# Performance work log

Measured on AMD Instinct MI355X. Metric: run time of the kernel, lower is better.

## Reference

```python
import jax, jax.numpy as jnp
import numpy as np

B, H, W, C, NH, K = 4, 56, 56, 128, 4, 7


def setup_inputs() -> dict:
    key = jax.random.key(0)
    ks = jax.random.split(key, 6)
    x = jax.random.normal(ks[0], (B, H, W, C), dtype=jnp.float32)
    w_qkv = jax.random.normal(ks[1], (C, 3 * C), dtype=jnp.float32) * 0.02
    b_qkv = jnp.zeros((3 * C,), dtype=jnp.float32)
    rpb = jax.random.normal(ks[2], (NH, 2 * K - 1, 2 * K - 1), dtype=jnp.float32) * 0.02
    w_proj = jax.random.normal(ks[3], (C, C), dtype=jnp.float32) * 0.02
    b_proj = jnp.zeros((C,), dtype=jnp.float32)
    return {"x": x, "w_qkv": w_qkv, "b_qkv": b_qkv, "rpb": rpb,
            "w_proj": w_proj, "b_proj": b_proj}


def reference(x, w_qkv, b_qkv, rpb, w_proj, b_proj):
    B_, H_, W_, C_ = x.shape
    nh = rpb.shape[0]
    k = (rpb.shape[1] + 1) // 2          # kernel_size
    hd = C_ // nh                        # head_dim
    nb = k // 2                          # neighborhood radius
    scale = hd ** -0.5

    qkv = (x @ w_qkv + b_qkv).reshape(B_, H_, W_, 3, nh, hd)
    q = qkv[:, :, :, 0].transpose(0, 3, 1, 2, 4) * scale   # [B,nh,H,W,hd]
    kk = qkv[:, :, :, 1].transpose(0, 3, 1, 2, 4)          # [B,nh,H,W,hd]
    v = qkv[:, :, :, 2].transpose(0, 3, 1, 2, 4)           # [B,nh,H,W,hd]

    # NATTEN window start indices: window clamped to stay in-bounds (query shifts off-center at edges)
    si = jnp.clip(jnp.arange(H_) - nb, 0, H_ - k)          # [H]
    sj = jnp.clip(jnp.arange(W_) - nb, 0, W_ - k)          # [W]
    idx_i = si[:, None] + jnp.arange(k)                    # [H,k] absolute key rows
    idx_j = sj[:, None] + jnp.arange(k)                    # [W,k] absolute key cols

    # gather neighborhood keys/values: [B,nh,H,k,W,k,hd] (axes: b n i p j q d)
    k_win = kk[:, :, idx_i][:, :, :, :, idx_j]
    v_win = v[:, :, idx_i][:, :, :, :, idx_j]

    # relative position bias: index = key_pos - query_pos + (k-1)
    rel_i = idx_i - jnp.arange(H_)[:, None] + (k - 1)      # [H,k]
    rel_j = idx_j - jnp.arange(W_)[:, None] + (k - 1)      # [W,k]
    bias = rpb[:, rel_i][:, :, :, rel_j]                   # [nh,H,k,W,k]
    bias = bias.transpose(0, 1, 3, 2, 4)                   # [nh,H,W,k,k]

    attn = jnp.einsum('bnijd,bnipjqd->bnijpq', q, k_win) + bias[None]
    attn = jax.nn.softmax(attn.reshape(B_, nh, H_, W_, k * k), axis=-1)
    attn = attn.reshape(B_, nh, H_, W_, k, k)

    out = jnp.einsum('bnijpq,bnipjqd->bnijd', attn, v_win)  # [B,nh,H,W,hd]
    out = out.transpose(0, 2, 3, 1, 4).reshape(B_, H_, W_, C_)
    return out @ w_proj + b_proj
```

## Files before the change

### kernel.cpp

```cpp
#include <hip/hip_runtime.h>

#define BATCH 4
#define HH 56
#define WW 56
#define CC 128
#define NHD 4
#define HD 32
#define KS 7
#define NB 3
#define HWSZ (HH * WW)
#define RPBW 13
#define QKV_N 384
#define QKV_ELE ((size_t)BATCH * NHD * HWSZ * HD)

__global__ __launch_bounds__(256) void qkv_gemm(
    const float* __restrict__ x, const float* __restrict__ w,
    const float* __restrict__ bias,
    float* __restrict__ qb, float* __restrict__ kb, float* __restrict__ vb)
{
    __shared__ float As[32][68];
    __shared__ float Bs[32][132];

    const int tid = threadIdx.x;
    const int tx  = tid & 15;
    const int ty  = tid >> 4;
    const int m0  = blockIdx.x * 64;
    const int n0  = blockIdx.y * 128;

    float acc[4][8];
    {
        const float4 ba = *(const float4*)(bias + n0 + 4 * tx);
        const float4 bb = *(const float4*)(bias + n0 + 64 + 4 * tx);
        #pragma unroll
        for (int i = 0; i < 4; ++i) {
            acc[i][0] = ba.x; acc[i][1] = ba.y; acc[i][2] = ba.z; acc[i][3] = ba.w;
            acc[i][4] = bb.x; acc[i][5] = bb.y; acc[i][6] = bb.z; acc[i][7] = bb.w;
        }
    }

    for (int kc = 0; kc < 128; kc += 32) {
        #pragma unroll
        for (int t = tid; t < 512; t += 256) {
            const int row = t >> 3;
            const int k4  = t & 7;
            const float4 xv = *(const float4*)(x + (size_t)(m0 + row) * CC + kc + 4 * k4);
            As[4 * k4 + 0][row] = xv.x;
            As[4 * k4 + 1][row] = xv.y;
            As[4 * k4 + 2][row] = xv.z;
            As[4 * k4 + 3][row] = xv.w;
        }
        #pragma unroll
        for (int t = tid; t < 1024; t += 256) {
            const int kr = t >> 5;
            const int n4 = t & 31;
            *(float4*)&Bs[kr][4 * n4] =
                *(const float4*)(w + (size_t)(kc + kr) * QKV_N + n0 + 4 * n4);
        }
        __syncthreads();
        #pragma unroll
        for (int kk = 0; kk < 32; ++kk) {
            const float4 a0 = *(const float4*)&As[kk][4 * ty];
            const float4 b0 = *(const float4*)&Bs[kk][4 * tx];
            const float4 b1 = *(const float4*)&Bs[kk][64 + 4 * tx];
            const float av[4] = {a0.x, a0.y, a0.z, a0.w};
            const float bv[8] = {b0.x, b0.y, b0.z, b0.w, b1.x, b1.y, b1.z, b1.w};
            #pragma unroll
            for (int i = 0; i < 4; ++i)
                #pragma unroll
                for (int j = 0; j < 8; ++j)
                    acc[i][j] += av[i] * bv[j];
        }
        __syncthreads();
    }

    const int t     = n0 >> 7;
    float* dst      = (t == 0) ? qb : (t == 1) ? kb : vb;
    const float scl = (t == 0) ? 0.17677669529663687f : 1.0f;
    const int c0 = 4 * tx;
    const int c1 = 64 + 4 * tx;
    const int h0 = c0 >> 5, d0 = c0 & 31;
    const int h1 = c1 >> 5, d1 = c1 & 31;
    const int b  = m0 / HWSZ;
    #pragma unroll
    for (int i = 0; i < 4; ++i) {
        const int m  = m0 + 4 * ty + i;
        const int ij = m - b * HWSZ;
        float* p0 = dst + ((size_t)(b * NHD + h0) * HWSZ + ij) * HD + d0;
        float* p1 = dst + ((size_t)(b * NHD + h1) * HWSZ + ij) * HD + d1;
        *(float4*)p0 = make_float4(acc[i][0] * scl, acc[i][1] * scl,
                                   acc[i][2] * scl, acc[i][3] * scl);
        *(float4*)p1 = make_float4(acc[i][4] * scl, acc[i][5] * scl,
                                   acc[i][6] * scl, acc[i][7] * scl);
    }
}

__global__ __launch_bounds__(256) void natten_attn(
    const float* __restrict__ qb, const float* __restrict__ kb,
    const float* __restrict__ vb, const float* __restrict__ rpb,
    float* __restrict__ ob)
{
    __shared__ float4 Ks[8][197];
    __shared__ float4 Vs[8][197];
    __shared__ float rpbs[RPBW * RPBW];

    const int tid = threadIdx.x;
    const int qid = tid >> 2;
    const int sub = tid & 3;
    const int qi_l = qid >> 3;
    const int qj_l = qid & 7;
    const int ti = blockIdx.x / 7;
    const int tj = blockIdx.x % 7;
    const int head = blockIdx.y;
    const int b    = blockIdx.z;
    const int qi = ti * 8 + qi_l;
    const int qj = tj * 8 + qj_l;
    const int R0 = min(max(ti * 8 - NB, 0), HH - 14);
    const int C0 = min(max(tj * 8 - NB, 0), WW - 14);

    const size_t base = (size_t)(b * NHD + head) * HWSZ;

    if (tid < RPBW * RPBW) rpbs[tid] = rpb[head * (RPBW * RPBW) + tid];

    for (int idx = tid; idx < 1568; idx += 256) {
        const int pos = idx >> 3;
        const int c   = idx & 7;
        const int ri  = pos / 14;
        const int rj  = pos - ri * 14;
        const size_t g = (base + (size_t)(R0 + ri) * WW + (C0 + rj)) * HD;
        Ks[c][pos] = ((const float4*)(kb + g))[c];
        Vs[c][pos] = ((const float4*)(vb + g))[c];
    }

    const int c0 = sub * 2;
    const float4* qp = (const float4*)(qb + (base + (size_t)qi * WW + qj) * HD) + c0;
    const float4 q0 = qp[0];
    const float4 q1 = qp[1];

    const int si  = min(max(qi - NB, 0), HH - KS);
    const int sj  = min(max(qj - NB, 0), WW - KS);
    const int ri0 = si - R0;
    const int rj0 = sj - C0;
    const int oi  = si - qi + (KS - 1);
    const int oj  = sj - qj + (KS - 1);

    __syncthreads();

    float s[49];
    #pragma unroll
    for (int pi = 0; pi < 7; ++pi) {
        const int rowoff = (ri0 + pi) * 14 + rj0;
        const int boff   = (oi + pi) * RPBW + oj;
        #pragma unroll
        for (int pj = 0; pj < 7; ++pj) {
            const int pos = rowoff + pj;
            const float4 k0 = Ks[c0][pos];
            const float4 k1 = Ks[c0 + 1][pos];
            float d = q0.x * k0.x + q0.y * k0.y + q0.z * k0.z + q0.w * k0.w
                    + q1.x * k1.x + q1.y * k1.y + q1.z * k1.z + q1.w * k1.w;
            d += __shfl_xor(d, 1, 64);
            d += __shfl_xor(d, 2, 64);
            s[pi * 7 + pj] = d + rpbs[boff + pj];
        }
    }

    float m = s[0];
    #pragma unroll
    for (int p = 1; p < 49; ++p) m = fmaxf(m, s[p]);
    float l = 0.f;
    #pragma unroll
    for (int p = 0; p < 49; ++p) { s[p] = __expf(s[p] - m); l += s[p]; }
    const float inv = 1.f / l;

    float4 o0 = make_float4(0.f, 0.f, 0.f, 0.f);
    float4 o1 = make_float4(0.f, 0.f, 0.f, 0.f);
    #pragma unroll
    for (int pi = 0; pi < 7; ++pi) {
        const int rowoff = (ri0 + pi) * 14 + rj0;
        #pragma unroll
        for (int pj = 0; pj < 7; ++pj) {
            const int pos = rowoff + pj;
            const float wt = s[pi * 7 + pj];
            const float4 v0 = Vs[c0][pos];
            const float4 v1 = Vs[c0 + 1][pos];
            o0.x += wt * v0.x; o0.y += wt * v0.y; o0.z += wt * v0.z; o0.w += wt * v0.w;
            o1.x += wt * v1.x; o1.y += wt * v1.y; o1.z += wt * v1.z; o1.w += wt * v1.w;
        }
    }

    float* op = ob + ((size_t)b * HWSZ + (size_t)qi * WW + qj) * CC + head * HD + sub * 8;
    ((float4*)op)[0] = make_float4(o0.x * inv, o0.y * inv, o0.z * inv, o0.w * inv);
    ((float4*)op)[1] = make_float4(o1.x * inv, o1.y * inv, o1.z * inv, o1.w * inv);
}

__global__ __launch_bounds__(256) void proj_gemm(
    const float* __restrict__ a, const float* __restrict__ w,
    const float* __restrict__ bias, float* __restrict__ out)
{
    __shared__ float As[32][36];
    __shared__ float Bs[32][132];

    const int tid = threadIdx.x;
    const int tx  = tid & 15;
    const int ty  = tid >> 4;
    const int m0  = blockIdx.x * 32;

    float acc[2][8];
    {
        const float4 ba = *(const float4*)(bias + 4 * tx);
        const float4 bb = *(const float4*)(bias + 64 + 4 * tx);
        #pragma unroll
        for (int i = 0; i < 2; ++i) {
            acc[i][0] = ba.x; acc[i][1] = ba.y; acc[i][2] = ba.z; acc[i][3] = ba.w;
            acc[i][4] = bb.x; acc[i][5] = bb.y; acc[i][6] = bb.z; acc[i][7] = bb.w;
        }
    }

    for (int kc = 0; kc < 128; kc += 32) {
        {
            const int row = tid >> 3;
            const int k4  = tid & 7;
            const float4 xv = *(const float4*)(a + (size_t)(m0 + row) * CC + kc + 4 * k4);
            As[4 * k4 + 0][row] = xv.x;
            As[4 * k4 + 1][row] = xv.y;
            As[4 * k4 + 2][row] = xv.z;
            As[4 * k4 + 3][row] = xv.w;
        }
        #pragma unroll
        for (int t = tid; t < 1024; t += 256) {
            const int kr = t >> 5;
            const int n4 = t & 31;
            *(float4*)&Bs[kr][4 * n4] =
                *(const float4*)(w + (size_t)(kc + kr) * CC + 4 * n4);
        }
        __syncthreads();
        #pragma unroll
        for (int kk = 0; kk < 32; ++kk) {
            const float2 a0 = *(const float2*)&As[kk][2 * ty];
            const float4 b0 = *(const float4*)&Bs[kk][4 * tx];
            const float4 b1 = *(const float4*)&Bs[kk][64 + 4 * tx];
            const float av[2] = {a0.x, a0.y};
            const float bv[8] = {b0.x, b0.y, b0.z, b0.w, b1.x, b1.y, b1.z, b1.w};
            #pragma unroll
            for (int i = 0; i < 2; ++i)
                #pragma unroll
                for (int j = 0; j < 8; ++j)
                    acc[i][j] += av[i] * bv[j];
        }
        __syncthreads();
    }

    #pragma unroll
    for (int i = 0; i < 2; ++i) {
        const int m = m0 + 2 * ty + i;
        float* p = out + (size_t)m * CC;
        *(float4*)(p + 4 * tx)      = make_float4(acc[i][0], acc[i][1], acc[i][2], acc[i][3]);
        *(float4*)(p + 64 + 4 * tx) = make_float4(acc[i][4], acc[i][5], acc[i][6], acc[i][7]);
    }
}

extern "C" void kernel_launch(void* const* d_in, const int* in_sizes, int n_in,
                              void* d_out, int out_size, void* d_ws, size_t ws_size,
                              hipStream_t stream) {
    const float* x      = (const float*)d_in[0];
    const float* w_qkv  = (const float*)d_in[1];
    const float* b_qkv  = (const float*)d_in[2];
    const float* rpb    = (const float*)d_in[3];
    const float* w_proj = (const float*)d_in[4];
    const float* b_proj = (const float*)d_in[5];
    float* out = (float*)d_out;

    float* ws  = (float*)d_ws;
    float* qbf = ws;
    float* kbf = ws + QKV_ELE;
    float* vbf = ws + 2 * QKV_ELE;
    float* obf = ws + 3 * QKV_ELE;

    qkv_gemm<<<dim3(196, 3), 256, 0, stream>>>(x, w_qkv, b_qkv, qbf, kbf, vbf);
    natten_attn<<<dim3(49, NHD, BATCH), 256, 0, stream>>>(qbf, kbf, vbf, rpb, obf);
    proj_gemm<<<392, 256, 0, stream>>>(obf, w_proj, b_proj, out);
}
```

Measured before the change: 127.5 us.

## Replace shared-memory tiled GEMMs with column-per-thread register GEMMs

```diff
diff --git a/kernel.cpp b/kernel.cpp
--- a/kernel.cpp
+++ b/kernel.cpp
@@ -13,84 +13,50 @@
 #define QKV_N 384
 #define QKV_ELE ((size_t)BATCH * NHD * HWSZ * HD)
 
-__global__ __launch_bounds__(256) void qkv_gemm(
+__global__ __launch_bounds__(384) void qkv_gemm(
     const float* __restrict__ x, const float* __restrict__ w,
     const float* __restrict__ bias,
     float* __restrict__ qb, float* __restrict__ kb, float* __restrict__ vb)
 {
-    __shared__ float As[32][68];
-    __shared__ float Bs[32][132];
-
-    const int tid = threadIdx.x;
-    const int tx  = tid & 15;
-    const int ty  = tid >> 4;
-    const int m0  = blockIdx.x * 64;
-    const int n0  = blockIdx.y * 128;
-
-    float acc[4][8];
-    {
-        const float4 ba = *(const float4*)(bias + n0 + 4 * tx);
-        const float4 bb = *(const float4*)(bias + n0 + 64 + 4 * tx);
-        #pragma unroll
-        for (int i = 0; i < 4; ++i) {
-            acc[i][0] = ba.x; acc[i][1] = ba.y; acc[i][2] = ba.z; acc[i][3] = ba.w;
-            acc[i][4] = bb.x; acc[i][5] = bb.y; acc[i][6] = bb.z; acc[i][7] = bb.w;
-        }
-    }
-
-    for (int kc = 0; kc < 128; kc += 32) {
-        #pragma unroll
-        for (int t = tid; t < 512; t += 256) {
-            const int row = t >> 3;
-            const int k4  = t & 7;
-            const float4 xv = *(const float4*)(x + (size_t)(m0 + row) * CC + kc + 4 * k4);
-            As[4 * k4 + 0][row] = xv.x;
-            As[4 * k4 + 1][row] = xv.y;
-            As[4 * k4 + 2][row] = xv.z;
-            As[4 * k4 + 3][row] = xv.w;
-        }
-        #pragma unroll
-        for (int t = tid; t < 1024; t += 256) {
-            const int kr = t >> 5;
-            const int n4 = t & 31;
-            *(float4*)&Bs[kr][4 * n4] =
-                *(const float4*)(w + (size_t)(kc + kr) * QKV_N + n0 + 4 * n4);
-        }
-        __syncthreads();
-        #pragma unroll
-        for (int kk = 0; kk < 32; ++kk) {
-            const float4 a0 = *(const float4*)&As[kk][4 * ty];
-            const float4 b0 = *(const float4*)&Bs[kk][4 * tx];
-            const float4 b1 = *(const float4*)&Bs[kk][64 + 4 * tx];
-            const float av[4] = {a0.x, a0.y, a0.z, a0.w};
-            const float bv[8] = {b0.x, b0.y, b0.z, b0.w, b1.x, b1.y, b1.z, b1.w};
-            #pragma unroll
-            for (int i = 0; i < 4; ++i)
-                #pragma unroll
-                for (int j = 0; j < 8; ++j)
-                    acc[i][j] += av[i] * bv[j];
-        }
-        __syncthreads();
-    }
-
-    const int t     = n0 >> 7;
-    float* dst      = (t == 0) ? qb : (t == 1) ? kb : vb;
+    const int col = threadIdx.x;
+    const int m0  = blockIdx.x * 16;
+
+    float acc[16];
+    const float bv = bias[col];
+    #pragma unroll
+    for (int r = 0; r < 16; ++r) acc[r] = bv;
+
+    const float* xrow = x + (size_t)m0 * CC;
+    const float* wc   = w + col;
+
+    for (int k4 = 0; k4 < 32; ++k4) {
+        const float w0 = wc[(k4 * 4 + 0) * QKV_N];
+        const float w1 = wc[(k4 * 4 + 1) * QKV_N];
+        const float w2 = wc[(k4 * 4 + 2) * QKV_N];
+        const float w3 = wc[(k4 * 4 + 3) * QKV_N];
+        #pragma unroll
+        for (int r = 0; r < 16; ++r) {
+            const float4 xv = *(const float4*)(xrow + (size_t)r * CC + k4 * 4);
+            acc[r] = fmaf(xv.x, w0, acc[r]);
+            acc[r] = fmaf(xv.y, w1, acc[r]);
+            acc[r] = fmaf(xv.z, w2, acc[r]);
+            acc[r] = fmaf(xv.w, w3, acc[r]);
+        }
+    }
+
+    const int t    = col >> 7;
+    const int rem  = col & 127;
+    const int head = rem >> 5;
+    const int d    = rem & 31;
     const float scl = (t == 0) ? 0.17677669529663687f : 1.0f;
-    const int c0 = 4 * tx;
-    const int c1 = 64 + 4 * tx;
-    const int h0 = c0 >> 5, d0 = c0 & 31;
-    const int h1 = c1 >> 5, d1 = c1 & 31;
-    const int b  = m0 / HWSZ;
-    #pragma unroll
-    for (int i = 0; i < 4; ++i) {
-        const int m  = m0 + 4 * ty + i;
-        const int ij = m - b * HWSZ;
-        float* p0 = dst + ((size_t)(b * NHD + h0) * HWSZ + ij) * HD + d0;
-        float* p1 = dst + ((size_t)(b * NHD + h1) * HWSZ + ij) * HD + d1;
-        *(float4*)p0 = make_float4(acc[i][0] * scl, acc[i][1] * scl,
-                                   acc[i][2] * scl, acc[i][3] * scl);
-        *(float4*)p1 = make_float4(acc[i][4] * scl, acc[i][5] * scl,
-                                   acc[i][6] * scl, acc[i][7] * scl);
+    float* dst = (t == 0) ? qb : (t == 1) ? kb : vb;
+
+    const int b   = m0 / HWSZ;
+    const int ij0 = m0 - b * HWSZ;
+    float* dsth = dst + (size_t)(b * NHD + head) * HWSZ * HD + d;
+    #pragma unroll
+    for (int r = 0; r < 16; ++r) {
+        dsth[(size_t)(ij0 + r) * HD] = acc[r] * scl;
     }
 }
 
@@ -192,70 +158,39 @@
     ((float4*)op)[1] = make_float4(o1.x * inv, o1.y * inv, o1.z * inv, o1.w * inv);
 }
 
-__global__ __launch_bounds__(256) void proj_gemm(
+__global__ __launch_bounds__(128) void proj_gemm(
     const float* __restrict__ a, const float* __restrict__ w,
     const float* __restrict__ bias, float* __restrict__ out)
 {
-    __shared__ float As[32][36];
-    __shared__ float Bs[32][132];
-
-    const int tid = threadIdx.x;
-    const int tx  = tid & 15;
-    const int ty  = tid >> 4;
-    const int m0  = blockIdx.x * 32;
-
-    float acc[2][8];
-    {
-        const float4 ba = *(const float4*)(bias + 4 * tx);
-        const float4 bb = *(const float4*)(bias + 64 + 4 * tx);
-        #pragma unroll
-        for (int i = 0; i < 2; ++i) {
-            acc[i][0] = ba.x; acc[i][1] = ba.y; acc[i][2] = ba.z; acc[i][3] = ba.w;
-            acc[i][4] = bb.x; acc[i][5] = bb.y; acc[i][6] = bb.z; acc[i][7] = bb.w;
-        }
-    }
-
-    for (int kc = 0; kc < 128; kc += 32) {
-        {
-            const int row = tid >> 3;
-            const int k4  = tid & 7;
-            const float4 xv = *(const float4*)(a + (size_t)(m0 + row) * CC + kc + 4 * k4);
-            As[4 * k4 + 0][row] = xv.x;
-            As[4 * k4 + 1][row] = xv.y;
-            As[4 * k4 + 2][row] = xv.z;
-            As[4 * k4 + 3][row] = xv.w;
-        }
-        #pragma unroll
-        for (int t = tid; t < 1024; t += 256) {
-            const int kr = t >> 5;
-            const int n4 = t & 31;
-            *(float4*)&Bs[kr][4 * n4] =
-                *(const float4*)(w + (size_t)(kc + kr) * CC + 4 * n4);
-        }
-        __syncthreads();
-        #pragma unroll
-        for (int kk = 0; kk < 32; ++kk) {
-            const float2 a0 = *(const float2*)&As[kk][2 * ty];
-            const float4 b0 = *(const float4*)&Bs[kk][4 * tx];
-            const float4 b1 = *(const float4*)&Bs[kk][64 + 4 * tx];
-            const float av[2] = {a0.x, a0.y};
-            const float bv[8] = {b0.x, b0.y, b0.z, b0.w, b1.x, b1.y, b1.z, b1.w};
-            #pragma unroll
-            for (int i = 0; i < 2; ++i)
-                #pragma unroll
-                for (int j = 0; j < 8; ++j)
-                    acc[i][j] += av[i] * bv[j];
-        }
-        __syncthreads();
-    }
-
-    #pragma unroll
-    for (int i = 0; i < 2; ++i) {
-        const int m = m0 + 2 * ty + i;
-        float* p = out + (size_t)m * CC;
-        *(float4*)(p + 4 * tx)      = make_float4(acc[i][0], acc[i][1], acc[i][2], acc[i][3]);
-        *(float4*)(p + 64 + 4 * tx) = make_float4(acc[i][4], acc[i][5], acc[i][6], acc[i][7]);
-    }
+    const int col = threadIdx.x;
+    const int m0  = blockIdx.x * 16;
+
+    float acc[16];
+    const float bv = bias[col];
+    #pragma unroll
+    for (int r = 0; r < 16; ++r) acc[r] = bv;
+
+    const float* arow = a + (size_t)m0 * CC;
+    const float* wc   = w + col;
+
+    for (int k4 = 0; k4 < 32; ++k4) {
+        const float w0 = wc[(k4 * 4 + 0) * CC];
+        const float w1 = wc[(k4 * 4 + 1) * CC];
+        const float w2 = wc[(k4 * 4 + 2) * CC];
+        const float w3 = wc[(k4 * 4 + 3) * CC];
+        #pragma unroll
+        for (int r = 0; r < 16; ++r) {
+            const float4 av = *(const float4*)(arow + (size_t)r * CC + k4 * 4);
+            acc[r] = fmaf(av.x, w0, acc[r]);
+            acc[r] = fmaf(av.y, w1, acc[r]);
+            acc[r] = fmaf(av.z, w2, acc[r]);
+            acc[r] = fmaf(av.w, w3, acc[r]);
+        }
+    }
+
+    float* op = out + (size_t)m0 * CC + col;
+    #pragma unroll
+    for (int r = 0; r < 16; ++r) op[(size_t)r * CC] = acc[r];
 }
 
 extern "C" void kernel_launch(void* const* d_in, const int* in_sizes, int n_in,
@@ -275,7 +210,7 @@
     float* vbf = ws + 2 * QKV_ELE;
     float* obf = ws + 3 * QKV_ELE;
 
-    qkv_gemm<<<dim3(196, 3), 256, 0, stream>>>(x, w_qkv, b_qkv, qbf, kbf, vbf);
+    qkv_gemm<<<784, 384, 0, stream>>>(x, w_qkv, b_qkv, qbf, kbf, vbf);
     natten_attn<<<dim3(49, NHD, BATCH), 256, 0, stream>>>(qbf, kbf, vbf, rpb, obf);
-    proj_gemm<<<392, 256, 0, stream>>>(obf, w_proj, b_proj, out);
-}
+    proj_gemm<<<784, 128, 0, stream>>>(obf, w_proj, b_proj, out);
+}
```

New measurement: 148.3 us. 1.16x slower.

## Load full A tile once and stream weights directly from global in GEMMs

Applied to the files above, without the earlier changes.

```diff
diff --git a/kernel.cpp b/kernel.cpp
--- a/kernel.cpp
+++ b/kernel.cpp
@@ -18,8 +18,7 @@
     const float* __restrict__ bias,
     float* __restrict__ qb, float* __restrict__ kb, float* __restrict__ vb)
 {
-    __shared__ float As[32][68];
-    __shared__ float Bs[32][132];
+    __shared__ float As[128][68];
 
     const int tid = threadIdx.x;
     const int tx  = tid & 15;
@@ -27,6 +26,17 @@
     const int m0  = blockIdx.x * 64;
     const int n0  = blockIdx.y * 128;
 
+    #pragma unroll
+    for (int t = tid; t < 2048; t += 256) {
+        const int row = t >> 5;
+        const int k4  = t & 31;
+        const float4 xv = *(const float4*)(x + (size_t)(m0 + row) * CC + 4 * k4);
+        As[4 * k4 + 0][row] = xv.x;
+        As[4 * k4 + 1][row] = xv.y;
+        As[4 * k4 + 2][row] = xv.z;
+        As[4 * k4 + 3][row] = xv.w;
+    }
+
     float acc[4][8];
     {
         const float4 ba = *(const float4*)(bias + n0 + 4 * tx);
@@ -38,39 +48,22 @@
         }
     }
 
-    for (int kc = 0; kc < 128; kc += 32) {
-        #pragma unroll
-        for (int t = tid; t < 512; t += 256) {
-            const int row = t >> 3;
-            const int k4  = t & 7;
-            const float4 xv = *(const float4*)(x + (size_t)(m0 + row) * CC + kc + 4 * k4);
-            As[4 * k4 + 0][row] = xv.x;
-            As[4 * k4 + 1][row] = xv.y;
-            As[4 * k4 + 2][row] = xv.z;
-            As[4 * k4 + 3][row] = xv.w;
-        }
-        #pragma unroll
-        for (int t = tid; t < 1024; t += 256) {
-            const int kr = t >> 5;
-            const int n4 = t & 31;
-            *(float4*)&Bs[kr][4 * n4] =
-                *(const float4*)(w + (size_t)(kc + kr) * QKV_N + n0 + 4 * n4);
-        }
-        __syncthreads();
-        #pragma unroll
-        for (int kk = 0; kk < 32; ++kk) {
-            const float4 a0 = *(const float4*)&As[kk][4 * ty];
-            const float4 b0 = *(const float4*)&Bs[kk][4 * tx];
-            const float4 b1 = *(const float4*)&Bs[kk][64 + 4 * tx];
-            const float av[4] = {a0.x, a0.y, a0.z, a0.w};
-            const float bv[8] = {b0.x, b0.y, b0.z, b0.w, b1.x, b1.y, b1.z, b1.w};
+    __syncthreads();
+
+    const float* wp0 = w + n0 + 4 * tx;
+    const float* wp1 = w + n0 + 64 + 4 * tx;
+    #pragma unroll 4
+    for (int kk = 0; kk < 128; ++kk) {
+        const float4 b0 = *(const float4*)(wp0 + (size_t)kk * QKV_N);
+        const float4 b1 = *(const float4*)(wp1 + (size_t)kk * QKV_N);
+        const float4 a0 = *(const float4*)&As[kk][4 * ty];
+        const float av[4] = {a0.x, a0.y, a0.z, a0.w};
+        const float bv[8] = {b0.x, b0.y, b0.z, b0.w, b1.x, b1.y, b1.z, b1.w};
+        #pragma unroll
+        for (int i = 0; i < 4; ++i)
             #pragma unroll
-            for (int i = 0; i < 4; ++i)
-                #pragma unroll
-                for (int j = 0; j < 8; ++j)
-                    acc[i][j] += av[i] * bv[j];
-        }
-        __syncthreads();
+            for (int j = 0; j < 8; ++j)
+                acc[i][j] = fmaf(av[i], bv[j], acc[i][j]);
     }
 
     const int t     = n0 >> 7;
@@ -196,14 +189,24 @@
     const float* __restrict__ a, const float* __restrict__ w,
     const float* __restrict__ bias, float* __restrict__ out)
 {
-    __shared__ float As[32][36];
-    __shared__ float Bs[32][132];
+    __shared__ float As[128][36];
 
     const int tid = threadIdx.x;
     const int tx  = tid & 15;
     const int ty  = tid >> 4;
     const int m0  = blockIdx.x * 32;
 
+    #pragma unroll
+    for (int t = tid; t < 1024; t += 256) {
+        const int row = t >> 5;
+        const int k4  = t & 31;
+        const float4 xv = *(const float4*)(a + (size_t)(m0 + row) * CC + 4 * k4);
+        As[4 * k4 + 0][row] = xv.x;
+        As[4 * k4 + 1][row] = xv.y;
+        As[4 * k4 + 2][row] = xv.z;
+        As[4 * k4 + 3][row] = xv.w;
+    }
+
     float acc[2][8];
     {
         const float4 ba = *(const float4*)(bias + 4 * tx);
@@ -215,38 +218,22 @@
         }
     }
 
-    for (int kc = 0; kc < 128; kc += 32) {
-        {
-            const int row = tid >> 3;
-            const int k4  = tid & 7;
-            const float4 xv = *(const float4*)(a + (size_t)(m0 + row) * CC + kc + 4 * k4);
-            As[4 * k4 + 0][row] = xv.x;
-            As[4 * k4 + 1][row] = xv.y;
-            As[4 * k4 + 2][row] = xv.z;
-            As[4 * k4 + 3][row] = xv.w;
-        }
-        #pragma unroll
-        for (int t = tid; t < 1024; t += 256) {
-            const int kr = t >> 5;
-            const int n4 = t & 31;
-            *(float4*)&Bs[kr][4 * n4] =
-                *(const float4*)(w + (size_t)(kc + kr) * CC + 4 * n4);
-        }
-        __syncthreads();
-        #pragma unroll
-        for (int kk = 0; kk < 32; ++kk) {
-            const float2 a0 = *(const float2*)&As[kk][2 * ty];
-            const float4 b0 = *(const float4*)&Bs[kk][4 * tx];
-            const float4 b1 = *(const float4*)&Bs[kk][64 + 4 * tx];
-            const float av[2] = {a0.x, a0.y};
-            const float bv[8] = {b0.x, b0.y, b0.z, b0.w, b1.x, b1.y, b1.z, b1.w};
+    __syncthreads();
+
+    const float* wp0 = w + 4 * tx;
+    const float* wp1 = w + 64 + 4 * tx;
+    #pragma unroll 4
+    for (int kk = 0; kk < 128; ++kk) {
+        const float4 b0 = *(const float4*)(wp0 + (size_t)kk * CC);
+        const float4 b1 = *(const float4*)(wp1 + (size_t)kk * CC);
+        const float2 a0 = *(const float2*)&As[kk][2 * ty];
+        const float av[2] = {a0.x, a0.y};
+        const float bv[8] = {b0.x, b0.y, b0.z, b0.w, b1.x, b1.y, b1.z, b1.w};
+        #pragma unroll
+        for (int i = 0; i < 2; ++i)
             #pragma unroll
-            for (int i = 0; i < 2; ++i)
-                #pragma unroll
-                for (int j = 0; j < 8; ++j)
-                    acc[i][j] += av[i] * bv[j];
-        }
-        __syncthreads();
+            for (int j = 0; j < 8; ++j)
+                acc[i][j] = fmaf(av[i], bv[j], acc[i][j]);
     }
 
     #pragma unroll
```

Result: slower. 141.1 us (+10.7%).
